# Kernel optimization log

Measured on AMD Instinct MI355X. Metric: run time of the kernel, lower is better.

Reference implementation:

```python
import jax, jax.numpy as jnp
import numpy as np

# PCDRender constants (from init_kwargs / raster settings)
H, W = 500, 512          # img_size
KPP = 10                 # points_per_pixel
RADIUS = 0.005           # rasterization radius, NDC units
FX, FY = 575.0, 575.0    # K[0,0], K[1,1]
PX, PY = 256.0, 250.0    # K[0,2], K[1,2]
N_PTS = 8192
S_MIN = float(min(H, W)) # shorter side defines PyTorch3D NDC scale


def setup_inputs() -> dict:
    key = jax.random.key(0)
    k1, k2 = jax.random.split(key)
    xy = 0.4 * jax.random.normal(k1, (N_PTS, 2), dtype=jnp.float32)
    z = 1.5 + jax.random.uniform(k2, (N_PTS, 1), dtype=jnp.float32)  # z in [1.5, 2.5), in front of camera
    points = jnp.concatenate([xy, z], axis=1)
    features = jnp.ones((N_PTS, 3), jnp.float32)  # load_pcd: features = ones_like(pcd)
    return {"points": points, "features": features}


def _project_ndc(points):
    # opencv_to_pytorch3d flips X,Y (R=diag(-1,-1,1), t=0); PerspectiveCameras(in_ndc=False)
    # projects to screen pixels, then rasterizer maps screen -> PyTorch3D NDC
    # (shorter side spans [-1,1], +x left, +y up).
    x, y, z = points[:, 0], points[:, 1], points[:, 2]
    u = -FX * x / z + PX                    # screen x (pixels)
    v = -FY * y / z + PY                    # screen y (pixels)
    x_ndc = -(2.0 * u - W) / S_MIN
    y_ndc = -(2.0 * v - H) / S_MIN
    return x_ndc, y_ndc, z


def _render(points, features):
    x_ndc, y_ndc, z = _project_ndc(points)
    # NDC coords of pixel centers
    xs_pix = -(2.0 * (jnp.arange(W, dtype=jnp.float32) + 0.5) - W) / S_MIN  # [W]
    ys_pix = -(2.0 * (jnp.arange(H, dtype=jnp.float32) + 0.5) - H) / S_MIN  # [H]
    r2 = RADIUS * RADIUS

    def row(y_pix):
        # per-pixel squared NDC distance to every point: [W, N]
        dx = xs_pix[:, None] - x_ndc[None, :]
        dy = y_pix - y_ndc                                  # [N]
        d2 = dx * dx + (dy * dy)[None, :]
        valid = (d2 < r2) & (z[None, :] > 0.0)
        keyz = jnp.where(valid, z[None, :], jnp.inf)
        # z-buffer top-k: KPP nearest-in-depth covering points, sorted front-to-back
        negz, idx = jax.lax.top_k(-keyz, KPP)               # [W, KPP]
        zsel = -negz
        ok = jnp.isfinite(zsel)
        d2sel = jnp.take_along_axis(d2, idx, axis=1)
        # weights = 1 - dists2 / r^2  (forward body), zero for empty slots
        wts = jnp.where(ok, 1.0 - d2sel / r2, 0.0)
        # AlphaCompositor (background 0): out = sum_k w_k * prod_{j<k}(1-w_j) * feat_k
        prev = jnp.concatenate(
            [jnp.ones((W, 1), wts.dtype), jnp.cumprod(1.0 - wts, axis=1)[:, :-1]], axis=1)
        feat = features[idx]                                # [W, KPP, 3]
        img_row = jnp.einsum('wk,wkc->wc', wts * prev, feat)
        zbuf_row = jnp.where(ok, zsel, -1.0)
        return img_row, zbuf_row

    imgs, zbuf = jax.lax.map(row, ys_pix)   # [H,W,3], [H,W,KPP]
    return imgs[None], zbuf[None]           # images [1,H,W,3], zbuf [1,H,W,KPP]


def reference(points, features):
    return _render(points, features)
```

## Files before the change

kernel.cpp:

```cpp
#include <hip/hip_runtime.h>

#define H_IMG   500
#define W_IMG   512
#define KPP     10
#define N_PTS   8192
#define TILE    16
#define TX_TILES 32
#define TY_TILES 32
#define N_TILES (TX_TILES * TY_TILES)
#define CAP     256
#define IMG_ELEMS (H_IMG * W_IMG * 3)

__global__ void pcd_bin_kernel(const float* __restrict__ pts,
                               float4* __restrict__ proj,
                               int* __restrict__ cnts,
                               int* __restrict__ lists) {
#pragma clang fp contract(off)
    int i = blockIdx.x * 256 + threadIdx.x;
    if (i >= N_PTS) return;

    float x = pts[i * 3 + 0];
    float y = pts[i * 3 + 1];
    float z = pts[i * 3 + 2];

    float u  = -575.0f * x / z + 256.0f;
    float v  = -575.0f * y / z + 250.0f;
    float xn = -(2.0f * u - 512.0f) / 500.0f;
    float yn = -(2.0f * v - 500.0f) / 500.0f;

    proj[i] = make_float4(xn, yn, z, __int_as_float(i));

    if (!(z > 0.0f)) return;

    const float R = 0.005f;
    float wlo_f = (511.0f - 500.0f * (xn + R)) * 0.5f - 1.0f;
    float whi_f = (511.0f - 500.0f * (xn - R)) * 0.5f + 1.0f;
    float hlo_f = (499.0f - 500.0f * (yn + R)) * 0.5f - 1.0f;
    float hhi_f = (499.0f - 500.0f * (yn - R)) * 0.5f + 1.0f;

    wlo_f = fmaxf(fminf(wlo_f, 1.0e6f), -1.0e6f);
    whi_f = fmaxf(fminf(whi_f, 1.0e6f), -1.0e6f);
    hlo_f = fmaxf(fminf(hlo_f, 1.0e6f), -1.0e6f);
    hhi_f = fmaxf(fminf(hhi_f, 1.0e6f), -1.0e6f);

    int wlo = max(0, (int)floorf(wlo_f));
    int whi = min(W_IMG - 1, (int)ceilf(whi_f));
    int hlo = max(0, (int)floorf(hlo_f));
    int hhi = min(H_IMG - 1, (int)ceilf(hhi_f));
    if (wlo > whi || hlo > hhi) return;

    int tx0 = wlo >> 4, tx1 = whi >> 4;
    int ty0 = hlo >> 4, ty1 = hhi >> 4;
    for (int ty = ty0; ty <= ty1; ++ty) {
        for (int tx = tx0; tx <= tx1; ++tx) {
            int t = ty * TX_TILES + tx;
            int pos = atomicAdd(&cnts[t], 1);
            if (pos < CAP) lists[t * CAP + pos] = i;
        }
    }
}

__global__ void pcd_render_kernel(const float4* __restrict__ proj,
                                  const int* __restrict__ cnts,
                                  const int* __restrict__ lists,
                                  const float* __restrict__ feats,
                                  float* __restrict__ out) {
#pragma clang fp contract(off)
    __shared__ float4 sp[CAP];

    int tile = blockIdx.x;
    int n = cnts[tile];
    n = n < CAP ? n : CAP;

    for (int j = threadIdx.x; j < n; j += 256) {
        sp[j] = proj[lists[tile * CAP + j]];
    }
    __syncthreads();

    int tx = threadIdx.x & 15;
    int ty = threadIdx.x >> 4;
    int w = (tile % TX_TILES) * TILE + tx;
    int h = (tile / TX_TILES) * TILE + ty;

    float xs = -(2.0f * ((float)w + 0.5f) - 512.0f) / 500.0f;
    float ys = -(2.0f * ((float)h + 0.5f) - 500.0f) / 500.0f;

    const float R2 = 0.005f * 0.005f;

    float zk[KPP];
    float dk[KPP];
    int   ik[KPP];
#pragma unroll
    for (int k = 0; k < KPP; ++k) { zk[k] = __builtin_inff(); dk[k] = 0.0f; ik[k] = 0x7fffffff; }

    for (int j = 0; j < n; ++j) {
        float4 p = sp[j];
        float dx = xs - p.x;
        float dy = ys - p.y;
        float dx2 = dx * dx;
        float dy2 = dy * dy;
        float d2 = dx2 + dy2;
        if (d2 < R2) {
            float cz = p.z, cd = d2;
            int ci = __float_as_int(p.w);
#pragma unroll
            for (int k = 0; k < KPP; ++k) {
                bool lt = (cz < zk[k]) || (cz == zk[k] && ci < ik[k]);
                float tz = zk[k], td = dk[k];
                int ti = ik[k];
                if (lt) {
                    zk[k] = cz; dk[k] = cd; ik[k] = ci;
                    cz = tz; cd = td; ci = ti;
                }
            }
        }
    }

    if (h < H_IMG) {
        float T = 1.0f;
        float c0 = 0.0f, c1 = 0.0f, c2 = 0.0f;
        int base = h * W_IMG + w;
        float* zout = out + IMG_ELEMS + base * KPP;
#pragma unroll
        for (int k = 0; k < KPP; ++k) {
            bool ok = zk[k] < __builtin_inff();
            float wt = ok ? (1.0f - dk[k] / R2) : 0.0f;
            float a = wt * T;
            if (ok) {
                int fi = ik[k] * 3;
                c0 += a * feats[fi + 0];
                c1 += a * feats[fi + 1];
                c2 += a * feats[fi + 2];
            }
            T = T * (1.0f - wt);
            zout[k] = ok ? zk[k] : -1.0f;
        }
        out[base * 3 + 0] = c0;
        out[base * 3 + 1] = c1;
        out[base * 3 + 2] = c2;
    }
}

extern "C" void kernel_launch(void* const* d_in, const int* in_sizes, int n_in,
                              void* d_out, int out_size, void* d_ws, size_t ws_size,
                              hipStream_t stream) {
    const float* points = (const float*)d_in[0];
    const float* feats  = (const float*)d_in[1];
    float* out = (float*)d_out;

    float4* proj = (float4*)d_ws;
    int* cnts = (int*)((char*)d_ws + N_PTS * sizeof(float4));
    int* lists = cnts + N_TILES;

    hipMemsetAsync(cnts, 0, N_TILES * sizeof(int), stream);

    pcd_bin_kernel<<<(N_PTS + 255) / 256, 256, 0, stream>>>(points, proj, cnts, lists);
    pcd_render_kernel<<<N_TILES, 256, 0, stream>>>(proj, cnts, lists, feats, out);
}
```

Measured before the change: 35.94 us.

## Fuse binning into render kernel with per-tile point culling in shared memory

Replaces the separate memset, binning kernel and render kernel with one kernel. Each tile block scans all points, projects them, and keeps those inside the tile's NDC bounds plus radius and margin, appending them to a shared-memory list through shared atomics. This removes two launches, the memset and the global atomics and list traffic. In exchange every block reprojects all 8192 points, 1024 times the projection work. The shared-memory list order is also nondeterministic, though ties are resolved by index.

```diff
diff --git a/kernel.cpp b/kernel.cpp
--- a/kernel.cpp
+++ b/kernel.cpp
@@ -11,80 +11,57 @@
 #define CAP     256
 #define IMG_ELEMS (H_IMG * W_IMG * 3)
 
-__global__ void pcd_bin_kernel(const float* __restrict__ pts,
-                               float4* __restrict__ proj,
-                               int* __restrict__ cnts,
-                               int* __restrict__ lists) {
+__global__ __launch_bounds__(256) void pcd_fused_kernel(
+        const float* __restrict__ pts,
+        const float* __restrict__ feats,
+        float* __restrict__ out) {
 #pragma clang fp contract(off)
-    int i = blockIdx.x * 256 + threadIdx.x;
-    if (i >= N_PTS) return;
+    __shared__ float4 sp[CAP];
+    __shared__ int scnt;
 
-    float x = pts[i * 3 + 0];
-    float y = pts[i * 3 + 1];
-    float z = pts[i * 3 + 2];
+    const int tile = blockIdx.x;
+    const int w0 = (tile & (TX_TILES - 1)) * TILE;
+    const int h0 = (tile >> 5) * TILE;
 
-    float u  = -575.0f * x / z + 256.0f;
-    float v  = -575.0f * y / z + 250.0f;
-    float xn = -(2.0f * u - 512.0f) / 500.0f;
-    float yn = -(2.0f * v - 500.0f) / 500.0f;
+    if (threadIdx.x == 0) scnt = 0;
+    __syncthreads();
 
-    proj[i] = make_float4(xn, yn, z, __int_as_float(i));
-
-    if (!(z > 0.0f)) return;
+    const float xhi = -(2.0f * ((float)w0 + 0.5f) - 512.0f) / 500.0f;
+    const float xlo = -(2.0f * ((float)(w0 + TILE - 1) + 0.5f) - 512.0f) / 500.0f;
+    const float yhi = -(2.0f * ((float)h0 + 0.5f) - 500.0f) / 500.0f;
+    const float ylo = -(2.0f * ((float)(h0 + TILE - 1) + 0.5f) - 500.0f) / 500.0f;
 
     const float R = 0.005f;
-    float wlo_f = (511.0f - 500.0f * (xn + R)) * 0.5f - 1.0f;
-    float whi_f = (511.0f - 500.0f * (xn - R)) * 0.5f + 1.0f;
-    float hlo_f = (499.0f - 500.0f * (yn + R)) * 0.5f - 1.0f;
-    float hhi_f = (499.0f - 500.0f * (yn - R)) * 0.5f + 1.0f;
+    const float M = 2.0e-4f;
+    const float cxlo = xlo - R - M, cxhi = xhi + R + M;
+    const float cylo = ylo - R - M, cyhi = yhi + R + M;
 
-    wlo_f = fmaxf(fminf(wlo_f, 1.0e6f), -1.0e6f);
-    whi_f = fmaxf(fminf(whi_f, 1.0e6f), -1.0e6f);
-    hlo_f = fmaxf(fminf(hlo_f, 1.0e6f), -1.0e6f);
-    hhi_f = fmaxf(fminf(hhi_f, 1.0e6f), -1.0e6f);
-
-    int wlo = max(0, (int)floorf(wlo_f));
-    int whi = min(W_IMG - 1, (int)ceilf(whi_f));
-    int hlo = max(0, (int)floorf(hlo_f));
-    int hhi = min(H_IMG - 1, (int)ceilf(hhi_f));
-    if (wlo > whi || hlo > hhi) return;
-
-    int tx0 = wlo >> 4, tx1 = whi >> 4;
-    int ty0 = hlo >> 4, ty1 = hhi >> 4;
-    for (int ty = ty0; ty <= ty1; ++ty) {
-        for (int tx = tx0; tx <= tx1; ++tx) {
-            int t = ty * TX_TILES + tx;
-            int pos = atomicAdd(&cnts[t], 1);
-            if (pos < CAP) lists[t * CAP + pos] = i;
+    for (int i = threadIdx.x; i < N_PTS; i += 256) {
+        float x = pts[i * 3 + 0];
+        float y = pts[i * 3 + 1];
+        float z = pts[i * 3 + 2];
+        float u  = -575.0f * x / z + 256.0f;
+        float v  = -575.0f * y / z + 250.0f;
+        float xn = -(2.0f * u - 512.0f) / 500.0f;
+        float yn = -(2.0f * v - 500.0f) / 500.0f;
+        bool keep = (z > 0.0f) & (xn > cxlo) & (xn < cxhi) & (yn > cylo) & (yn < cyhi);
+        if (keep) {
+            int p = atomicAdd(&scnt, 1);
+            if (p < CAP) sp[p] = make_float4(xn, yn, z, __int_as_float(i));
         }
-    }
-}
-
-__global__ void pcd_render_kernel(const float4* __restrict__ proj,
-                                  const int* __restrict__ cnts,
-                                  const int* __restrict__ lists,
-                                  const float* __restrict__ feats,
-                                  float* __restrict__ out) {
-#pragma clang fp contract(off)
-    __shared__ float4 sp[CAP];
-
-    int tile = blockIdx.x;
-    int n = cnts[tile];
-    n = n < CAP ? n : CAP;
-
-    for (int j = threadIdx.x; j < n; j += 256) {
-        sp[j] = proj[lists[tile * CAP + j]];
     }
     __syncthreads();
 
-    int tx = threadIdx.x & 15;
-    int ty = threadIdx.x >> 4;
-    int w = (tile % TX_TILES) * TILE + tx;
-    int h = (tile / TX_TILES) * TILE + ty;
+    int n = scnt;
+    n = n < CAP ? n : CAP;
 
-    float xs = -(2.0f * ((float)w + 0.5f) - 512.0f) / 500.0f;
-    float ys = -(2.0f * ((float)h + 0.5f) - 500.0f) / 500.0f;
+    const int tx = threadIdx.x & 15;
+    const int ty = threadIdx.x >> 4;
+    const int w = w0 + tx;
+    const int h = h0 + ty;
 
+    const float xs = -(2.0f * ((float)w + 0.5f) - 512.0f) / 500.0f;
+    const float ys = -(2.0f * ((float)h + 0.5f) - 500.0f) / 500.0f;
     const float R2 = 0.005f * 0.005f;
 
     float zk[KPP];
@@ -119,7 +96,7 @@
     if (h < H_IMG) {
         float T = 1.0f;
         float c0 = 0.0f, c1 = 0.0f, c2 = 0.0f;
-        int base = h * W_IMG + w;
+        const int base = h * W_IMG + w;
         float* zout = out + IMG_ELEMS + base * KPP;
 #pragma unroll
         for (int k = 0; k < KPP; ++k) {
@@ -147,13 +124,7 @@
     const float* points = (const float*)d_in[0];
     const float* feats  = (const float*)d_in[1];
     float* out = (float*)d_out;
+    (void)d_ws; (void)ws_size;
 
-    float4* proj = (float4*)d_ws;
-    int* cnts = (int*)((char*)d_ws + N_PTS * sizeof(float4));
-    int* lists = cnts + N_TILES;
-
-    hipMemsetAsync(cnts, 0, N_TILES * sizeof(int), stream);
-
-    pcd_bin_kernel<<<(N_PTS + 255) / 256, 256, 0, stream>>>(points, proj, cnts, lists);
-    pcd_render_kernel<<<N_TILES, 256, 0, stream>>>(proj, cnts, lists, feats, out);
+    pcd_fused_kernel<<<N_TILES, 256, 0, stream>>>(points, feats, out);
 }
```

New measurement: 37.44 us. 4.2% more time.

## Bin point and feature data directly per tile and stage outputs in shared memory

Applied to the files above, without the earlier changes.

The bin kernel now writes the projected position and the feature vector straight into per-tile float4 arrays. This removes the indirect index list, the gather through proj, and the per-pixel global feature lookups in the render kernel. The render kernel keeps a slot index into shared features, uses a branchless insertion into named registers, and stages zbuf and image rows in shared memory so the global stores are coalesced. In exchange the bin kernel writes twice as much data per binned point, the render kernel uses more shared memory, and the padded tile rows beyond the image are now computed before being masked at store time.

```diff
diff --git a/kernel.cpp b/kernel.cpp
--- a/kernel.cpp
+++ b/kernel.cpp
@@ -11,13 +11,40 @@
 #define CAP     256
 #define IMG_ELEMS (H_IMG * W_IMG * 3)
 
-__global__ void pcd_bin_kernel(const float* __restrict__ pts,
-                               float4* __restrict__ proj,
-                               int* __restrict__ cnts,
-                               int* __restrict__ lists) {
+
+#define INSERT(ZZ, DD, II, SS)                                         \
+    {                                                                  \
+        bool lt = (cz < ZZ) || ((cz == ZZ) && (ci < II));              \
+        float tz = ZZ, td = DD; int ti = II, ts = SS;                  \
+        ZZ = lt ? cz : ZZ;  DD = lt ? cd : DD;                         \
+        II = lt ? ci : II;  SS = lt ? cs : SS;                         \
+        cz = lt ? tz : cz;  cd = lt ? td : cd;                         \
+        ci = lt ? ti : ci;  cs = lt ? ts : cs;                         \
+    }
+
+#define EMIT(K, ZZ, DD, SS)                                            \
+    {                                                                  \
+        bool ok = ZZ < __builtin_inff();                               \
+        float wt = ok ? (1.0f - DD / R2) : 0.0f;                       \
+        float a = wt * T;                                              \
+        if (ok) {                                                      \
+            float4 f = sf[SS];                                         \
+            c0 += a * f.x;                                             \
+            c1 += a * f.y;                                             \
+            c2 += a * f.z;                                             \
+        }                                                              \
+        T = T * (1.0f - wt);                                           \
+        szb[ty][tx * KPP + K] = ok ? ZZ : -1.0f;                       \
+    }
+
+__global__ __launch_bounds__(256) void pcd_bin_kernel(
+        const float* __restrict__ pts,
+        const float* __restrict__ feats,
+        int* __restrict__ cnts,
+        float4* __restrict__ posArr,
+        float4* __restrict__ featArr) {
 #pragma clang fp contract(off)
     int i = blockIdx.x * 256 + threadIdx.x;
-    if (i >= N_PTS) return;
 
     float x = pts[i * 3 + 0];
     float y = pts[i * 3 + 1];
@@ -27,8 +54,6 @@
     float v  = -575.0f * y / z + 250.0f;
     float xn = -(2.0f * u - 512.0f) / 500.0f;
     float yn = -(2.0f * v - 500.0f) / 500.0f;
-
-    proj[i] = make_float4(xn, yn, z, __int_as_float(i));
 
     if (!(z > 0.0f)) return;
 
@@ -48,6 +73,9 @@
     int hlo = max(0, (int)floorf(hlo_f));
     int hhi = min(H_IMG - 1, (int)ceilf(hhi_f));
     if (wlo > whi || hlo > hhi) return;
+
+    float4 pe = make_float4(xn, yn, z, __int_as_float(i));
+    float4 fe = make_float4(feats[i * 3 + 0], feats[i * 3 + 1], feats[i * 3 + 2], 0.0f);
 
     int tx0 = wlo >> 4, tx1 = whi >> 4;
     int ty0 = hlo >> 4, ty1 = hhi >> 4;
@@ -55,43 +83,56 @@
         for (int tx = tx0; tx <= tx1; ++tx) {
             int t = ty * TX_TILES + tx;
             int pos = atomicAdd(&cnts[t], 1);
-            if (pos < CAP) lists[t * CAP + pos] = i;
+            if (pos < CAP) {
+                posArr[t * CAP + pos] = pe;
+                featArr[t * CAP + pos] = fe;
+            }
         }
     }
 }
 
-__global__ void pcd_render_kernel(const float4* __restrict__ proj,
-                                  const int* __restrict__ cnts,
-                                  const int* __restrict__ lists,
-                                  const float* __restrict__ feats,
-                                  float* __restrict__ out) {
+__global__ __launch_bounds__(256) void pcd_render_kernel(
+        const int* __restrict__ cnts,
+        const float4* __restrict__ posArr,
+        const float4* __restrict__ featArr,
+        float* __restrict__ out) {
 #pragma clang fp contract(off)
     __shared__ float4 sp[CAP];
-
-    int tile = blockIdx.x;
+    __shared__ float4 sf[CAP];
+    __shared__ float szb[TILE][TILE * KPP + 1];
+    __shared__ float simg[TILE][TILE * 3 + 1];
+
+    const int tile = blockIdx.x;
+    const int w0 = (tile & (TX_TILES - 1)) * TILE;
+    const int h0 = (tile >> 5) * TILE;
+
     int n = cnts[tile];
     n = n < CAP ? n : CAP;
 
     for (int j = threadIdx.x; j < n; j += 256) {
-        sp[j] = proj[lists[tile * CAP + j]];
+        sp[j] = posArr[tile * CAP + j];
+        sf[j] = featArr[tile * CAP + j];
     }
     __syncthreads();
 
-    int tx = threadIdx.x & 15;
-    int ty = threadIdx.x >> 4;
-    int w = (tile % TX_TILES) * TILE + tx;
-    int h = (tile / TX_TILES) * TILE + ty;
-
-    float xs = -(2.0f * ((float)w + 0.5f) - 512.0f) / 500.0f;
-    float ys = -(2.0f * ((float)h + 0.5f) - 500.0f) / 500.0f;
-
+    const int tx = threadIdx.x & 15;
+    const int ty = threadIdx.x >> 4;
+    const int w = w0 + tx;
+    const int h = h0 + ty;
+
+    const float xs = -(2.0f * ((float)w + 0.5f) - 512.0f) / 500.0f;
+    const float ys = -(2.0f * ((float)h + 0.5f) - 500.0f) / 500.0f;
     const float R2 = 0.005f * 0.005f;
-
-    float zk[KPP];
-    float dk[KPP];
-    int   ik[KPP];
-#pragma unroll
-    for (int k = 0; k < KPP; ++k) { zk[k] = __builtin_inff(); dk[k] = 0.0f; ik[k] = 0x7fffffff; }
+    const float INF = __builtin_inff();
+
+    float kz0 = INF, kz1 = INF, kz2 = INF, kz3 = INF, kz4 = INF;
+    float kz5 = INF, kz6 = INF, kz7 = INF, kz8 = INF, kz9 = INF;
+    float kd0 = 0, kd1 = 0, kd2 = 0, kd3 = 0, kd4 = 0;
+    float kd5 = 0, kd6 = 0, kd7 = 0, kd8 = 0, kd9 = 0;
+    int ki0 = 0x7fffffff, ki1 = 0x7fffffff, ki2 = 0x7fffffff, ki3 = 0x7fffffff, ki4 = 0x7fffffff;
+    int ki5 = 0x7fffffff, ki6 = 0x7fffffff, ki7 = 0x7fffffff, ki8 = 0x7fffffff, ki9 = 0x7fffffff;
+    int ks0 = 0, ks1 = 0, ks2 = 0, ks3 = 0, ks4 = 0;
+    int ks5 = 0, ks6 = 0, ks7 = 0, ks8 = 0, ks9 = 0;
 
     for (int j = 0; j < n; ++j) {
         float4 p = sp[j];
@@ -103,41 +144,52 @@
         if (d2 < R2) {
             float cz = p.z, cd = d2;
             int ci = __float_as_int(p.w);
-#pragma unroll
-            for (int k = 0; k < KPP; ++k) {
-                bool lt = (cz < zk[k]) || (cz == zk[k] && ci < ik[k]);
-                float tz = zk[k], td = dk[k];
-                int ti = ik[k];
-                if (lt) {
-                    zk[k] = cz; dk[k] = cd; ik[k] = ci;
-                    cz = tz; cd = td; ci = ti;
-                }
-            }
+            int cs = j;
+            INSERT(kz0, kd0, ki0, ks0);
+            INSERT(kz1, kd1, ki1, ks1);
+            INSERT(kz2, kd2, ki2, ks2);
+            INSERT(kz3, kd3, ki3, ks3);
+            INSERT(kz4, kd4, ki4, ks4);
+            INSERT(kz5, kd5, ki5, ks5);
+            INSERT(kz6, kd6, ki6, ks6);
+            INSERT(kz7, kd7, ki7, ks7);
+            INSERT(kz8, kd8, ki8, ks8);
+            INSERT(kz9, kd9, ki9, ks9);
         }
     }
 
-    if (h < H_IMG) {
+    {
         float T = 1.0f;
         float c0 = 0.0f, c1 = 0.0f, c2 = 0.0f;
-        int base = h * W_IMG + w;
-        float* zout = out + IMG_ELEMS + base * KPP;
-#pragma unroll
-        for (int k = 0; k < KPP; ++k) {
-            bool ok = zk[k] < __builtin_inff();
-            float wt = ok ? (1.0f - dk[k] / R2) : 0.0f;
-            float a = wt * T;
-            if (ok) {
-                int fi = ik[k] * 3;
-                c0 += a * feats[fi + 0];
-                c1 += a * feats[fi + 1];
-                c2 += a * feats[fi + 2];
-            }
-            T = T * (1.0f - wt);
-            zout[k] = ok ? zk[k] : -1.0f;
-        }
-        out[base * 3 + 0] = c0;
-        out[base * 3 + 1] = c1;
-        out[base * 3 + 2] = c2;
+        EMIT(0, kz0, kd0, ks0);
+        EMIT(1, kz1, kd1, ks1);
+        EMIT(2, kz2, kd2, ks2);
+        EMIT(3, kz3, kd3, ks3);
+        EMIT(4, kz4, kd4, ks4);
+        EMIT(5, kz5, kd5, ks5);
+        EMIT(6, kz6, kd6, ks6);
+        EMIT(7, kz7, kd7, ks7);
+        EMIT(8, kz8, kd8, ks8);
+        EMIT(9, kz9, kd9, ks9);
+        simg[ty][tx * 3 + 0] = c0;
+        simg[ty][tx * 3 + 1] = c1;
+        simg[ty][tx * 3 + 2] = c2;
+    }
+    __syncthreads();
+
+    for (int e = threadIdx.x; e < TILE * TILE * KPP; e += 256) {
+        int r = e / (TILE * KPP);
+        int c = e - r * (TILE * KPP);
+        int hh = h0 + r;
+        if (hh < H_IMG)
+            out[IMG_ELEMS + (hh * W_IMG + w0) * KPP + c] = szb[r][c];
+    }
+    for (int e = threadIdx.x; e < TILE * TILE * 3; e += 256) {
+        int r = e / (TILE * 3);
+        int c = e - r * (TILE * 3);
+        int hh = h0 + r;
+        if (hh < H_IMG)
+            out[(hh * W_IMG + w0) * 3 + c] = simg[r][c];
     }
 }
 
@@ -148,12 +200,11 @@
     const float* feats  = (const float*)d_in[1];
     float* out = (float*)d_out;
 
-    float4* proj = (float4*)d_ws;
-    int* cnts = (int*)((char*)d_ws + N_PTS * sizeof(float4));
-    int* lists = cnts + N_TILES;
+    int* cnts = (int*)d_ws;
+    float4* posArr  = (float4*)((char*)d_ws + 4096);
+    float4* featArr = (float4*)((char*)d_ws + 4096 + N_TILES * CAP * 16);
 
     hipMemsetAsync(cnts, 0, N_TILES * sizeof(int), stream);
-
-    pcd_bin_kernel<<<(N_PTS + 255) / 256, 256, 0, stream>>>(points, proj, cnts, lists);
-    pcd_render_kernel<<<N_TILES, 256, 0, stream>>>(proj, cnts, lists, feats, out);
+    pcd_bin_kernel<<<N_PTS / 256, 256, 0, stream>>>(points, feats, cnts, posArr, featArr);
+    pcd_render_kernel<<<N_TILES, 256, 0, stream>>>(cnts, posArr, featArr, out);
 }
```

Result: faster. 34.70 us (-3.4%).
